# Performance work log

Measured on AMD Instinct MI355X. Metric: run time of the kernel, lower is better.

Reference implementation:

```python
import jax, jax.numpy as jnp
import numpy as np

N_NODES = 100000
N_EDGES = 1600000

def gcn_conv(x, src, dst, W, b, n):
    # symmetric GCN normalization with self-loops already included in src/dst
    deg = jax.ops.segment_sum(jnp.ones_like(src, dtype=x.dtype), dst, num_segments=n)
    dinv = jnp.where(deg > 0, jax.lax.rsqrt(deg), 0.0)
    norm = dinv[src] * dinv[dst]            # [E]
    h = x @ W                                # [n, out]
    msg = h[src] * norm[:, None]             # gather + scale, [E, out]
    out = jax.ops.segment_sum(msg, dst, num_segments=n)  # scatter-add
    return out + b

def setup_inputs() -> dict:
    key = jax.random.key(0)
    k1, k2, k3, k4 = jax.random.split(key, 4)
    x = jax.random.normal(k1, (N_NODES, 768), dtype=jnp.float32)
    edge_index = jax.random.randint(k2, (2, N_EDGES), 0, N_NODES, dtype=jnp.int64)
    W1 = jax.random.normal(k3, (768, 64), dtype=jnp.float32) * (1.0 / np.sqrt(768))
    b1 = jnp.zeros((64,), dtype=jnp.float32)
    W2 = jax.random.normal(k4, (64, 32), dtype=jnp.float32) * (1.0 / np.sqrt(64))
    b2 = jnp.zeros((32,), dtype=jnp.float32)
    return {"x": x, "edge_index": edge_index, "W1": W1, "b1": b1, "W2": W2, "b2": b2}

def reference(x, edge_index, W1, b1, W2, b2):
    n = x.shape[0]
    loop = jnp.arange(n, dtype=edge_index.dtype)
    src = jnp.concatenate([edge_index[0], loop])
    dst = jnp.concatenate([edge_index[1], loop])
    h = jax.nn.relu(gcn_conv(x, src, dst, W1, b1, n))
    # F.dropout with training=False -> identity (eval mode)
    out = gcn_conv(h, src, dst, W2, b2, n)
    return out
```

## Files before the change

kernel.cpp:

```cpp
#include <hip/hip_runtime.h>


constexpr int C1 = 64;
constexpr int C2 = 32;
constexpr int K1 = 768;
constexpr int SCAN_BS = 256;
constexpr int SCAN_ELEMS = 2048;

typedef __attribute__((ext_vector_type(8))) short short8;
typedef __attribute__((ext_vector_type(4))) float floatx4;

__global__ void detect_k(const int* __restrict__ ei32, int* flag, int n_words) {
    __shared__ int any_nz;
    if (threadIdx.x == 0) any_nz = 0;
    __syncthreads();
    int w = 2 * threadIdx.x + 1;
    if (w < n_words && ei32[w] != 0) atomicOr(&any_nz, 1);
    __syncthreads();
    if (threadIdx.x == 0) *flag = (any_nz == 0) ? 1 : 0;
}

__device__ __forceinline__ int load_idx(const void* ei, size_t pos, int m64) {
    if (m64) return (int)((const long long*)ei)[pos];
    return ((const int*)ei)[pos];
}

__global__ void zero_k(int* p, int n) {
    int i = blockIdx.x * 256 + threadIdx.x;
    if (i < n) p[i] = 0;
}

__global__ void cnt_k(const void* __restrict__ ei, const int* __restrict__ flag,
                      int* cnt, int E) {
    int e = blockIdx.x * 256 + threadIdx.x;
    if (e >= E) return;
    int m64 = *flag;
    int d = load_idx(ei, (size_t)E + e, m64);
    atomicAdd(&cnt[d], 1);
}

__global__ void dinv_k(const int* __restrict__ cnt, float* dinv, int n) {
    int i = blockIdx.x * 256 + threadIdx.x;
    if (i < n) dinv[i] = rsqrtf(1.0f + (float)cnt[i]);
}

__global__ void scan1_k(const int* __restrict__ cnt, int* partials, int n) {
    __shared__ int s[SCAN_BS];
    int base = blockIdx.x * SCAN_ELEMS;
    int t = threadIdx.x;
    int sum = 0;
    #pragma unroll
    for (int i = 0; i < 8; ++i) {
        int idx = base + t * 8 + i;
        if (idx < n) sum += cnt[idx];
    }
    s[t] = sum;
    __syncthreads();
    for (int off = 128; off > 0; off >>= 1) {
        if (t < off) s[t] += s[t + off];
        __syncthreads();
    }
    if (t == 0) partials[blockIdx.x] = s[0];
}

__global__ void scan2_k(int* partials, int* total_out, int nb) {
    __shared__ int s[256];
    int t = threadIdx.x;
    int v = (t < nb) ? partials[t] : 0;
    s[t] = v;
    __syncthreads();
    for (int off = 1; off < 256; off <<= 1) {
        int add = (t >= off) ? s[t - off] : 0;
        __syncthreads();
        s[t] += add;
        __syncthreads();
    }
    if (t < nb) partials[t] = s[t] - v;
    if (t == 0) *total_out = s[255];
}

__global__ void scan3_k(const int* __restrict__ cnt, const int* __restrict__ partials,
                        int* offsets, int* cursor, int n) {
    __shared__ int s[SCAN_BS];
    int base = blockIdx.x * SCAN_ELEMS;
    int t = threadIdx.x;
    int local[8];
    int sum = 0;
    #pragma unroll
    for (int i = 0; i < 8; ++i) {
        int idx = base + t * 8 + i;
        int v = (idx < n) ? cnt[idx] : 0;
        local[i] = sum;
        sum += v;
    }
    int mine = sum;
    s[t] = sum;
    __syncthreads();
    for (int off = 1; off < 256; off <<= 1) {
        int add = (t >= off) ? s[t - off] : 0;
        __syncthreads();
        s[t] += add;
        __syncthreads();
    }
    int texcl = s[t] - mine;
    int boff = partials[blockIdx.x];
    #pragma unroll
    for (int i = 0; i < 8; ++i) {
        int idx = base + t * 8 + i;
        if (idx < n) {
            int o = boff + texcl + local[i];
            offsets[idx] = o;
            cursor[idx] = o;
        }
    }
}

__global__ void fill_k(const void* __restrict__ ei, const int* __restrict__ flag,
                       int* cursor, int* adj, int E) {
    int e = blockIdx.x * 256 + threadIdx.x;
    if (e >= E) return;
    int m64 = *flag;
    int s = load_idx(ei, e, m64);
    int d = load_idx(ei, (size_t)E + e, m64);
    int pos = atomicAdd(&cursor[d], 1);
    adj[pos] = s;
}

__device__ __forceinline__ void bf16_split(float f, unsigned short& hi, unsigned short& lo) {
    unsigned int u = __float_as_uint(f);
    unsigned int r1 = (u + 0x7FFFu + ((u >> 16) & 1u)) & 0xFFFF0000u;
    hi = (unsigned short)(r1 >> 16);
    float rem = f - __uint_as_float(r1);
    unsigned int u2 = __float_as_uint(rem);
    lo = (unsigned short)((u2 + 0x7FFFu + ((u2 >> 16) & 1u)) >> 16);
}

__global__ void packW1_k(const float* __restrict__ W1, unsigned short* __restrict__ Bp) {
    int gid = blockIdx.x * 256 + threadIdx.x;
    if (gid >= 24 * 4 * 2 * 64) return;
    int l    = gid & 63;
    int frag = gid >> 6;
    int p = frag & 1;
    int t = (frag >> 1) & 3;
    int s = frag >> 3;
    int c = t * 16 + (l & 15);
    int kbase = s * 32 + (l >> 4) * 8;
    short8 v;
    #pragma unroll
    for (int j = 0; j < 8; ++j) {
        unsigned short hi, lo;
        bf16_split(W1[(size_t)(kbase + j) * C1 + c], hi, lo);
        v[j] = (short)(p ? lo : hi);
    }
    *(short8*)(Bp + (size_t)gid * 8) = v;
}

__global__ __launch_bounds__(256) void gemm1_k(const float* __restrict__ x,
                                               const unsigned short* __restrict__ Bp,
                                               const float* __restrict__ dinv,
                                               float* __restrict__ g1, int n) {
    constexpr int MT = 128;
    __shared__ float As[MT * 32];
    const int tid = threadIdx.x;
    const int w = tid >> 6;
    const int l = tid & 63;
    const int block_row = blockIdx.x * MT;

    floatx4 zero = {0.f, 0.f, 0.f, 0.f};
    floatx4 acc[2][4];
    #pragma unroll
    for (int r = 0; r < 2; ++r)
        #pragma unroll
        for (int t = 0; t < 4; ++t) acc[r][t] = zero;

    const int srow = l >> 3;
    const int skb  = (l & 7) ^ srow;

    for (int s = 0; s < 24; ++s) {
        const int k0 = s * 32;
        #pragma unroll
        for (int gi = 0; gi < 4; ++gi) {
            int g = w * 4 + gi;
            int row = block_row + g * 8 + srow;
            if (row > n - 1) row = n - 1;
            const float* src = x + (size_t)row * K1 + k0 + skb * 4;
            float* ldst = &As[g * 256];
            __builtin_amdgcn_global_load_lds(
                (const __attribute__((address_space(1))) void*)src,
                (__attribute__((address_space(3))) void*)ldst, 16, 0, 0);
        }
        short8 bh[4], bl[4];
        #pragma unroll
        for (int t = 0; t < 4; ++t) {
            size_t fb = ((size_t)(s * 4 + t) * 2) * 512;
            bh[t] = *(const short8*)(Bp + fb + l * 8);
            bl[t] = *(const short8*)(Bp + fb + 512 + l * 8);
        }
        __syncthreads();
        #pragma unroll
        for (int r = 0; r < 2; ++r) {
            int row_local = w * 32 + r * 16 + (l & 15);
            int swz = l & 7;
            int kb0 = ((l >> 4) * 2) ^ swz;
            floatx4 f0 = *(const floatx4*)&As[row_local * 32 + kb0 * 4];
            floatx4 f1 = *(const floatx4*)&As[row_local * 32 + (kb0 ^ 1) * 4];
            short8 ah, al;
            float fv[8] = {f0[0], f0[1], f0[2], f0[3], f1[0], f1[1], f1[2], f1[3]};
            #pragma unroll
            for (int j = 0; j < 8; ++j) {
                unsigned short h16, l16;
                bf16_split(fv[j], h16, l16);
                ah[j] = (short)h16;
                al[j] = (short)l16;
            }
            #pragma unroll
            for (int t = 0; t < 4; ++t) {
                acc[r][t] = __builtin_amdgcn_mfma_f32_16x16x32_bf16(ah, bh[t], acc[r][t], 0, 0, 0);
                acc[r][t] = __builtin_amdgcn_mfma_f32_16x16x32_bf16(al, bh[t], acc[r][t], 0, 0, 0);
                acc[r][t] = __builtin_amdgcn_mfma_f32_16x16x32_bf16(ah, bl[t], acc[r][t], 0, 0, 0);
            }
        }
        __syncthreads();
    }

    #pragma unroll
    for (int r = 0; r < 2; ++r) {
        #pragma unroll
        for (int i = 0; i < 4; ++i) {
            int row = block_row + w * 32 + r * 16 + (l >> 4) * 4 + i;
            if (row < n) {
                float dv = dinv[row];
                #pragma unroll
                for (int t = 0; t < 4; ++t) {
                    g1[(size_t)row * C1 + t * 16 + (l & 15)] = acc[r][t][i] * dv;
                }
            }
        }
    }
}

__global__ __launch_bounds__(256) void gather1_k(const int* __restrict__ offsets,
                                                 const int* __restrict__ adj,
                                                 const float* __restrict__ dinv,
                                                 const float* __restrict__ g1,
                                                 const float* __restrict__ b1,
                                                 const float* __restrict__ W2,
                                                 float* __restrict__ g2, int n) {
    __shared__ float sW[C1 * C2];
    __shared__ float srow[4][C1];
    const int tid = threadIdx.x;
    for (int i = tid; i < C1 * C2; i += 256) sW[i] = W2[i];

    const int wid = tid >> 6;
    const int c = tid & 63;
    const int v = blockIdx.x * 4 + wid;

    float r = 0.f;
    float dv = 0.f;
    if (v < n) {
        dv = dinv[v];
        int start = offsets[v], end = offsets[v + 1];
        float acc = g1[(size_t)v * C1 + c];
        int j = start;
        for (; j + 4 <= end; j += 4) {
            int s0 = adj[j], s1 = adj[j + 1], s2 = adj[j + 2], s3 = adj[j + 3];
            float a0 = g1[(size_t)s0 * C1 + c];
            float a1 = g1[(size_t)s1 * C1 + c];
            float a2 = g1[(size_t)s2 * C1 + c];
            float a3 = g1[(size_t)s3 * C1 + c];
            acc += (a0 + a1) + (a2 + a3);
        }
        for (; j < end; ++j) acc += g1[(size_t)adj[j] * C1 + c];
        r = fmaxf(b1[c] + dv * acc, 0.f);
    }
    srow[wid][c] = r;
    __syncthreads();

    if (v < n && c < C2) {
        float acc = 0.f;
        #pragma unroll
        for (int k = 0; k < C1; ++k) acc += srow[wid][k] * sW[k * C2 + c];
        g2[(size_t)v * C2 + c] = dv * acc;
    }
}

__global__ __launch_bounds__(256) void gather2_k(const int* __restrict__ offsets,
                                                 const int* __restrict__ adj,
                                                 const float* __restrict__ dinv,
                                                 const float* __restrict__ g2,
                                                 const float* __restrict__ b2,
                                                 float* __restrict__ out, int n) {
    int v = blockIdx.x * 8 + (threadIdx.x >> 5);
    int c = threadIdx.x & 31;
    if (v >= n) return;
    int start = offsets[v], end = offsets[v + 1];
    float acc = g2[(size_t)v * C2 + c];
    int j = start;
    for (; j + 4 <= end; j += 4) {
        int s0 = adj[j], s1 = adj[j + 1], s2 = adj[j + 2], s3 = adj[j + 3];
        float a0 = g2[(size_t)s0 * C2 + c];
        float a1 = g2[(size_t)s1 * C2 + c];
        float a2 = g2[(size_t)s2 * C2 + c];
        float a3 = g2[(size_t)s3 * C2 + c];
        acc += (a0 + a1) + (a2 + a3);
    }
    for (; j < end; ++j) acc += g2[(size_t)adj[j] * C2 + c];
    out[(size_t)v * C2 + c] = b2[c] + dinv[v] * acc;
}

extern "C" void kernel_launch(void* const* d_in, const int* in_sizes, int n_in,
                              void* d_out, int out_size, void* d_ws, size_t ws_size,
                              hipStream_t stream) {
    const float* x  = (const float*)d_in[0];
    const void*  ei = d_in[1];
    const float* W1 = (const float*)d_in[2];
    const float* b1 = (const float*)d_in[3];
    const float* W2 = (const float*)d_in[4];
    const float* b2 = (const float*)d_in[5];
    float* out = (float*)d_out;

    const int n = in_sizes[0] / K1;
    const int E = in_sizes[1] / 2;

    float* ws      = (float*)d_ws;
    int*   flag    = (int*)ws;
    float* dinv    = ws + 16;
    float* g1      = dinv + n;
    float* g2      = g1 + (size_t)n * C1;
    int*   cnt     = (int*)(g2 + (size_t)n * C2);
    int*   offsets = cnt + n;
    int*   cursor  = offsets + n + 1;
    int*   partials= cursor + n;
    int*   adj     = partials + 256;
    uintptr_t bp_a = ((uintptr_t)(adj + E) + 15) & ~(uintptr_t)15;
    unsigned short* Bp = (unsigned short*)bp_a;

    const int nb_scan = (n + SCAN_ELEMS - 1) / SCAN_ELEMS;

    detect_k<<<1, 256, 0, stream>>>((const int*)ei, flag, in_sizes[1]);
    zero_k<<<(n + 255) / 256, 256, 0, stream>>>(cnt, n);
    cnt_k<<<(E + 255) / 256, 256, 0, stream>>>(ei, flag, cnt, E);
    dinv_k<<<(n + 255) / 256, 256, 0, stream>>>(cnt, dinv, n);

    packW1_k<<<48, 256, 0, stream>>>(W1, Bp);
    gemm1_k<<<(n + 127) / 128, 256, 0, stream>>>(x, Bp, dinv, g1, n);

    scan1_k<<<nb_scan, SCAN_BS, 0, stream>>>(cnt, partials, n);
    scan2_k<<<1, 256, 0, stream>>>(partials, offsets + n, nb_scan);
    scan3_k<<<nb_scan, SCAN_BS, 0, stream>>>(cnt, partials, offsets, cursor, n);
    fill_k<<<(E + 255) / 256, 256, 0, stream>>>(ei, flag, cursor, adj, E);

    gather1_k<<<(n + 3) / 4, 256, 0, stream>>>(offsets, adj, dinv, g1, b1, W2, g2, n);
    gather2_k<<<(n + 7) / 8, 256, 0, stream>>>(offsets, adj, dinv, g2, b2, out, n);
}
```

Before: 801.3 us.

## Double-buffer A and B tiles in LDS for gemm1 with async prefetch

The first-layer GEMM now stages both the x tile and the packed W1 fragments into double-buffered LDS with global_load_lds. It issues the next k-step's loads before computing the current one and waits with a partial vmcnt. The bf16 hi/lo split is simplified by truncating the low part instead of rounding it, and by reusing the rounded word. This aims to overlap global memory latency with the MFMA work and to trim VALU cost. In exchange it uses more LDS, which may lower occupancy, and the lo term carries slightly more rounding error.

New measurement: 816.7 us. About the same (+1.9%).

```diff
diff --git a/kernel.cpp b/kernel.cpp
--- a/kernel.cpp
+++ b/kernel.cpp
@@ -126,13 +126,12 @@
     adj[pos] = s;
 }
 
-__device__ __forceinline__ void bf16_split(float f, unsigned short& hi, unsigned short& lo) {
+__device__ __forceinline__ void bf16_split(float f, short& hi, short& lo) {
     unsigned int u = __float_as_uint(f);
-    unsigned int r1 = (u + 0x7FFFu + ((u >> 16) & 1u)) & 0xFFFF0000u;
-    hi = (unsigned short)(r1 >> 16);
-    float rem = f - __uint_as_float(r1);
-    unsigned int u2 = __float_as_uint(rem);
-    lo = (unsigned short)((u2 + 0x7FFFu + ((u2 >> 16) & 1u)) >> 16);
+    unsigned int r = u + (0x7FFFu + ((u >> 16) & 1u));
+    hi = (short)(r >> 16);
+    float rem = f - __uint_as_float(r & 0xFFFF0000u);
+    lo = (short)(__float_as_uint(rem) >> 16);
 }
 
 __global__ void packW1_k(const float* __restrict__ W1, unsigned short* __restrict__ Bp) {
@@ -148,9 +147,9 @@
     short8 v;
     #pragma unroll
     for (int j = 0; j < 8; ++j) {
-        unsigned short hi, lo;
+        short hi, lo;
         bf16_split(W1[(size_t)(kbase + j) * C1 + c], hi, lo);
-        v[j] = (short)(p ? lo : hi);
+        v[j] = p ? lo : hi;
     }
     *(short8*)(Bp + (size_t)gid * 8) = v;
 }
@@ -160,7 +159,8 @@
                                                const float* __restrict__ dinv,
                                                float* __restrict__ g1, int n) {
     constexpr int MT = 128;
-    __shared__ float As[MT * 32];
+    __shared__ alignas(16) float As[2][MT * 32];
+    __shared__ alignas(16) unsigned short Bs[2][4096];
     const int tid = threadIdx.x;
     const int w = tid >> 6;
     const int l = tid & 63;
@@ -176,7 +176,7 @@
     const int srow = l >> 3;
     const int skb  = (l & 7) ^ srow;
 
-    for (int s = 0; s < 24; ++s) {
+    auto stage = [&](int s, int b) {
         const int k0 = s * 32;
         #pragma unroll
         for (int gi = 0; gi < 4; ++gi) {
@@ -184,43 +184,64 @@
             int row = block_row + g * 8 + srow;
             if (row > n - 1) row = n - 1;
             const float* src = x + (size_t)row * K1 + k0 + skb * 4;
-            float* ldst = &As[g * 256];
             __builtin_amdgcn_global_load_lds(
                 (const __attribute__((address_space(1))) void*)src,
-                (__attribute__((address_space(3))) void*)ldst, 16, 0, 0);
-        }
+                (__attribute__((address_space(3))) void*)&As[b][g * 256], 16, 0, 0);
+        }
+        #pragma unroll
+        for (int gi = 0; gi < 2; ++gi) {
+            int j = w * 2 + gi;
+            const unsigned short* src = Bp + (size_t)s * 4096 + j * 512 + l * 8;
+            __builtin_amdgcn_global_load_lds(
+                (const __attribute__((address_space(1))) void*)src,
+                (__attribute__((address_space(3))) void*)&Bs[b][j * 512], 16, 0, 0);
+        }
+    };
+
+    stage(0, 0);
+
+    for (int t = 0; t < 24; ++t) {
+        int nxt = (t + 1 < 24) ? t + 1 : 23;
+        stage(nxt, (t + 1) & 1);
+
+        asm volatile("s_waitcnt vmcnt(6)" ::: "memory");
+        __builtin_amdgcn_s_barrier();
+
+        const float* A = As[t & 1];
+        const unsigned short* B = Bs[t & 1];
+
         short8 bh[4], bl[4];
         #pragma unroll
-        for (int t = 0; t < 4; ++t) {
-            size_t fb = ((size_t)(s * 4 + t) * 2) * 512;
-            bh[t] = *(const short8*)(Bp + fb + l * 8);
-            bl[t] = *(const short8*)(Bp + fb + 512 + l * 8);
-        }
-        __syncthreads();
+        for (int tt = 0; tt < 4; ++tt) {
+            bh[tt] = *(const short8*)(B + (tt * 2 + 0) * 512 + l * 8);
+            bl[tt] = *(const short8*)(B + (tt * 2 + 1) * 512 + l * 8);
+        }
+
         #pragma unroll
         for (int r = 0; r < 2; ++r) {
             int row_local = w * 32 + r * 16 + (l & 15);
             int swz = l & 7;
             int kb0 = ((l >> 4) * 2) ^ swz;
-            floatx4 f0 = *(const floatx4*)&As[row_local * 32 + kb0 * 4];
-            floatx4 f1 = *(const floatx4*)&As[row_local * 32 + (kb0 ^ 1) * 4];
+            floatx4 f0 = *(const floatx4*)&A[row_local * 32 + kb0 * 4];
+            floatx4 f1 = *(const floatx4*)&A[row_local * 32 + (kb0 ^ 1) * 4];
             short8 ah, al;
             float fv[8] = {f0[0], f0[1], f0[2], f0[3], f1[0], f1[1], f1[2], f1[3]};
             #pragma unroll
             for (int j = 0; j < 8; ++j) {
-                unsigned short h16, l16;
+                short h16, l16;
                 bf16_split(fv[j], h16, l16);
-                ah[j] = (short)h16;
-                al[j] = (short)l16;
+                ah[j] = h16;
+                al[j] = l16;
             }
             #pragma unroll
-            for (int t = 0; t < 4; ++t) {
-                acc[r][t] = __builtin_amdgcn_mfma_f32_16x16x32_bf16(ah, bh[t], acc[r][t], 0, 0, 0);
-                acc[r][t] = __builtin_amdgcn_mfma_f32_16x16x32_bf16(al, bh[t], acc[r][t], 0, 0, 0);
-                acc[r][t] = __builtin_amdgcn_mfma_f32_16x16x32_bf16(ah, bl[t], acc[r][t], 0, 0, 0);
+            for (int tt = 0; tt < 4; ++tt) {
+                acc[r][tt] = __builtin_amdgcn_mfma_f32_16x16x32_bf16(ah, bh[tt], acc[r][tt], 0, 0, 0);
+                acc[r][tt] = __builtin_amdgcn_mfma_f32_16x16x32_bf16(al, bh[tt], acc[r][tt], 0, 0, 0);
+                acc[r][tt] = __builtin_amdgcn_mfma_f32_16x16x32_bf16(ah, bl[tt], acc[r][tt], 0, 0, 0);
             }
         }
-        __syncthreads();
+
+        __builtin_amdgcn_s_barrier();
     }
 
     #pragma unroll
```
